# Performance work log

Hardware: AMD Instinct MI355X
Metric: run time of the kernel (lower is better)

Reference implementation:

```python
import jax, jax.numpy as jnp
import numpy as np

T = 16          # timesteps
BATCH = 8       # video clips -> leading dim of x is BATCH*T = 128
C_IN = 768      # fixed by nn.Conv2d(768, redu_dim, 1)
D = 256         # redu_dim
K = 64          # num_centers
H = W = 28
EPS = 1e-12     # torch F.normalize eps


def _conv(x, w, padding):
    # x: [N,C,H,W], w: [O,I,kh,kw]
    return jax.lax.conv_general_dilated(
        x, w, window_strides=(1, 1), padding=padding,
        dimension_numbers=('NCHW', 'OIHW', 'NCHW'))


def setup_inputs() -> dict:
    key = jax.random.key(0)
    ks = jax.random.split(key, 9)
    x = jax.random.normal(ks[0], (BATCH * T, C_IN, H, W), dtype=jnp.float32)
    redu_w = jax.random.normal(ks[1], (D, C_IN, 1, 1), jnp.float32) * 0.02
    redu_b = jnp.zeros((D,), jnp.float32)
    share_w = jax.random.normal(ks[2], (K, D, 1, 1), jnp.float32) * 0.05
    share_b = jnp.zeros((K,), jnp.float32)
    U_z = jax.random.normal(ks[3], (K, K, 3, 3), jnp.float32) * 0.04
    U_r = jax.random.normal(ks[4], (K, K, 3, 3), jnp.float32) * 0.04
    U_h = jax.random.normal(ks[5], (K, K, 3, 3), jnp.float32) * 0.04
    centers = jax.random.normal(ks[6], (K, D), jnp.float32) * 0.06
    return {"x": x, "redu_w": redu_w, "redu_b": redu_b,
            "share_w": share_w, "share_b": share_b,
            "U_z": U_z, "U_r": U_r, "U_h": U_h,
            "centers": centers, "timesteps": T}


def reference(x, redu_w, redu_b, share_w, share_b, U_z, U_r, U_h, centers, timesteps):
    t = timesteps
    bt, _, h, w = x.shape
    b = bt // t
    k = share_w.shape[0]
    d = redu_w.shape[0]

    # channel reduction (1x1 conv)
    xr = _conv(x, redu_w, 'VALID') + redu_b[None, :, None, None]        # [bt,d,h,w]
    # shared assignment logits (1x1 conv)
    wxb = _conv(xr, share_w, 'VALID') + share_b[None, :, None, None]     # [bt,k,h,w]
    wxb = wxb.reshape(b, t, k, h, w).transpose(1, 0, 2, 3, 4)            # [t,b,k,h,w]

    # sequential ConvGRU over timesteps
    h0 = jnp.zeros((b, k, h, w), x.dtype)
    def step(h_tm1, w_t):
        z = jax.nn.sigmoid(w_t + _conv(h_tm1, U_z, 'SAME'))
        r = jax.nn.sigmoid(w_t + _conv(h_tm1, U_r, 'SAME'))
        hh = jnp.tanh(w_t + _conv(r * h_tm1, U_h, 'SAME'))
        h_new = (1.0 - z) * hh + z * h_tm1
        return h_new, h_new
    _, hs = jax.lax.scan(step, h0, wxb)                                  # [t,b,k,h,w]

    assign = hs.transpose(1, 0, 2, 3, 4).reshape(b * t, k, h * w)        # [bt,k,hw]
    # softmax over centers per spatial location
    assign = jax.nn.softmax(assign, axis=1)

    # VLAD aggregation
    a_sum = assign.sum(axis=-1, keepdims=True)                           # [bt,k,1]
    a = a_sum * centers[None]                                            # [bt,k,d]
    xf = xr.reshape(b * t, d, h * w)                                     # [bt,d,hw]
    vlad = jnp.einsum('bkp,bdp->bkd', assign, xf) - a                    # [bt,k,d]

    vlad = vlad.reshape(b, t, k, d).sum(axis=1)                          # [b,k,d]
    # intra-norm over feature dim, then global L2 norm
    vlad = vlad / jnp.maximum(jnp.linalg.norm(vlad, axis=2, keepdims=True), EPS)
    vlad = vlad.reshape(b, k * d)
    vlad = vlad / jnp.maximum(jnp.linalg.norm(vlad, axis=1, keepdims=True), EPS)
    return vlad
```

## Files before the change

### kernel.cpp

```cpp
#include <hip/hip_runtime.h>
#include <hip/hip_bf16.h>

#define T_ 16
#define B_ 8
#define CIN 768
#define D_ 256
#define K_ 64
#define HW 784
#define W_ 28

typedef short short8 __attribute__((ext_vector_type(8)));
typedef short short4v __attribute__((ext_vector_type(4)));
typedef float floatx4 __attribute__((ext_vector_type(4)));
typedef unsigned short ushort_t;

__device__ __forceinline__ unsigned short f2bf(float x) {
    union { float f; unsigned u; } v; v.f = x;
    unsigned u = v.u;
    unsigned r = (u + 0x7fffu + ((u >> 16) & 1u)) >> 16;
    return (unsigned short)r;
}
__device__ __forceinline__ float bf2f(unsigned short h) {
    union { unsigned u; float f; } v; v.u = ((unsigned)h) << 16; return v.f;
}

__device__ __forceinline__ float block_reduce_sum_256(float v) {
    for (int off = 32; off > 0; off >>= 1) v += __shfl_down(v, off, 64);
    __shared__ float red[4];
    __shared__ float tot;
    int lane = threadIdx.x & 63, wid = threadIdx.x >> 6;
    if (lane == 0) red[wid] = v;
    __syncthreads();
    if (threadIdx.x == 0) tot = red[0] + red[1] + red[2] + red[3];
    __syncthreads();
    return tot;
}

__global__ __launch_bounds__(256) void cvt_weights(
    const float* __restrict__ rw, const float* __restrict__ sw,
    const float* __restrict__ Uz, const float* __restrict__ Ur,
    const float* __restrict__ Uh,
    ushort_t* __restrict__ whi, ushort_t* __restrict__ wlo,
    ushort_t* __restrict__ shi, ushort_t* __restrict__ slo,
    ushort_t* __restrict__ azh, ushort_t* __restrict__ azl,
    ushort_t* __restrict__ ahh, ushort_t* __restrict__ ahl)
{
    int i = blockIdx.x * 256 + threadIdx.x;
    const int nR = D_ * CIN;
    const int nS = K_ * D_;
    const int nZR = 128 * 576;
    const int nH = 64 * 576;
    if (i < nR) {
        float x = rw[i];
        unsigned short h = f2bf(x);
        whi[i] = h; wlo[i] = f2bf(x - bf2f(h));
    } else if (i < nR + nS) {
        int j = i - nR;
        float x = sw[j];
        unsigned short h = f2bf(x);
        shi[j] = h; slo[j] = f2bf(x - bf2f(h));
    } else if (i < nR + nS + nZR) {
        int j = i - nR - nS;
        int row = j / 576, kk = j - row * 576;
        int tap = kk >> 6, c = kk & 63;
        const float* U = (row < 64) ? Uz : Ur;
        float x = U[(((size_t)(row & 63)) * 64 + c) * 9 + tap];
        unsigned short h = f2bf(x);
        azh[j] = h; azl[j] = f2bf(x - bf2f(h));
    } else if (i < nR + nS + nZR + nH) {
        int j = i - nR - nS - nZR;
        int row = j / 576, kk = j - row * 576;
        int tap = kk >> 6, c = kk & 63;
        float x = Uh[(((size_t)row) * 64 + c) * 9 + tap];
        unsigned short h = f2bf(x);
        ahh[j] = h; ahl[j] = f2bf(x - bf2f(h));
    }
}

template<int BM, int THR, int KD>
__global__ __launch_bounds__(THR, 4) void mfma_conv1x1(
    const float* __restrict__ X, const ushort_t* __restrict__ Whi,
    const ushort_t* __restrict__ Wlo, const float* __restrict__ bias,
    float* __restrict__ Out)
{
    const int nt = blockIdx.x, bt = blockIdx.z;
    const int p0 = nt * 112;
    const int tid = threadIdx.x, lane = tid & 63, wv = tid >> 6;
    const int li = lane & 15, koff = (lane >> 4) * 8;
    constexpr int NWAVE = THR / 64;
    constexpr int MI = BM / (NWAVE * 16);
    constexpr int NKS = KD / 32;
    constexpr int UPT = (THR == 512) ? 1 : 2;
    const float* Xb = X + (size_t)bt * KD * HW;
    float* Ob = Out + (size_t)bt * BM * HW;

    __shared__ ushort_t lB[2][2][112 * 40];

    floatx4 acc[MI][7];
#pragma unroll
    for (int a = 0; a < MI; ++a)
#pragma unroll
        for (int b = 0; b < 7; ++b) acc[a][b] = (floatx4){0.f, 0.f, 0.f, 0.f};

    float bA[8 * UPT], bB[8 * UPT];
    short8 ahi[MI], alo[MI];

    auto loadB = [&](int k0, float* bb) {
#pragma unroll
        for (int u = 0; u < UPT; ++u) {
            int uu = tid + u * THR;
            if (uu < 448) {
                int j = uu / 112, pp = uu - j * 112;
                const float* xp = Xb + (size_t)(k0 + j * 8) * HW + p0 + pp;
#pragma unroll
                for (int c = 0; c < 8; ++c) bb[u * 8 + c] = xp[(size_t)c * HW];
            }
        }
    };
    auto writeB = [&](const float* bb, int wb) {
#pragma unroll
        for (int u = 0; u < UPT; ++u) {
            int uu = tid + u * THR;
            if (uu < 448) {
                int j = uu / 112, pp = uu - j * 112;
                short8 vh, vl;
#pragma unroll
                for (int c = 0; c < 8; ++c) {
                    unsigned short h = f2bf(bb[u * 8 + c]);
                    vh[c] = (short)h; vl[c] = (short)f2bf(bb[u * 8 + c] - bf2f(h));
                }
                *(short8*)&lB[wb][0][pp * 40 + j * 8] = vh;
                *(short8*)&lB[wb][1][pp * 40 + j * 8] = vl;
            }
        }
    };
    auto loadA = [&](int k0) {
#pragma unroll
        for (int mi = 0; mi < MI; ++mi) {
            int m = wv * (MI * 16) + mi * 16 + li;
            ahi[mi] = *(const short8*)(Whi + (size_t)m * KD + k0 + koff);
            alo[mi] = *(const short8*)(Wlo + (size_t)m * KD + k0 + koff);
        }
    };
    auto domfma = [&](int rb) {
        const ushort_t* bh = &lB[rb][0][0];
        const ushort_t* bl = &lB[rb][1][0];
#pragma unroll
        for (int ni = 0; ni < 7; ++ni) {
            int n = ni * 16 + li;
            short8 bhi = *(const short8*)&bh[n * 40 + koff];
            short8 blo = *(const short8*)&bl[n * 40 + koff];
#pragma unroll
            for (int mi = 0; mi < MI; ++mi) {
                acc[mi][ni] = __builtin_amdgcn_mfma_f32_16x16x32_bf16(ahi[mi], bhi, acc[mi][ni], 0, 0, 0);
                acc[mi][ni] = __builtin_amdgcn_mfma_f32_16x16x32_bf16(ahi[mi], blo, acc[mi][ni], 0, 0, 0);
                acc[mi][ni] = __builtin_amdgcn_mfma_f32_16x16x32_bf16(alo[mi], bhi, acc[mi][ni], 0, 0, 0);
            }
        }
    };

    loadB(0, bA);
    writeB(bA, 0);
    loadB(32, bB);
    __syncthreads();

    for (int ks = 0; ks < NKS; ks += 2) {
        loadA(ks * 32);
        if (ks + 1 < NKS) writeB(bB, 1);
        if (ks + 2 < NKS) loadB((ks + 2) * 32, bA);
        domfma(0);
        __syncthreads();
        loadA((ks + 1) * 32);
        if (ks + 2 < NKS) writeB(bA, 0);
        if (ks + 3 < NKS) loadB((ks + 3) * 32, bB);
        domfma(1);
        __syncthreads();
    }

#pragma unroll
    for (int mi = 0; mi < MI; ++mi) {
        int m0g = wv * (MI * 16) + mi * 16 + ((lane >> 4) << 2);
#pragma unroll
        for (int ni = 0; ni < 7; ++ni) {
            int p = p0 + ni * 16 + li;
#pragma unroll
            for (int r = 0; r < 4; ++r)
                Ob[(size_t)(m0g + r) * HW + p] = acc[mi][ni][r] + bias[m0g + r];
        }
    }
}

__global__ __launch_bounds__(512, 2) void gru_step(
    const ushort_t* __restrict__ hRhi, const ushort_t* __restrict__ hRlo,
    ushort_t* __restrict__ hWhi, ushort_t* __restrict__ hWlo,
    const ushort_t* __restrict__ azh, const ushort_t* __restrict__ azl,
    const ushort_t* __restrict__ ahh, const ushort_t* __restrict__ ahl,
    const float* __restrict__ wxb, float* __restrict__ hs_t, int t)
{
    const int y0 = blockIdx.x, b = blockIdx.y;
    const int tid = threadIdx.x, lane = tid & 63, wv = tid >> 6;
    const int li = lane & 15, koff8 = (lane >> 4) * 8, kq = (lane >> 4) * 4;

    __shared__ ushort_t Hhi[5 * 30 * 72], Hlo[5 * 30 * 72];
    __shared__ ushort_t Rhi[3 * 30 * 72], Rlo[3 * 30 * 72];
    __shared__ float zs[28 * 68];

    {
        const ushort_t* gh = hRhi + (size_t)b * HW * 64;
        const ushort_t* gl = hRlo + (size_t)b * HW * 64;
        for (int e = tid; e < 1200; e += 512) {
            int r = e / 240, rem = e - r * 240;
            int lx = rem >> 3, j = rem & 7;
            int gy = y0 - 2 + r, gx = lx - 1;
            short8 vh = {0,0,0,0,0,0,0,0}, vl = {0,0,0,0,0,0,0,0};
            if (gy >= 0 && gy < 28 && gx >= 0 && gx < 28) {
                size_t go = ((size_t)(gy * 28 + gx)) * 64 + j * 8;
                vh = *(const short8*)(gh + go);
                vl = *(const short8*)(gl + go);
            }
            int lo = (r * 30 + lx) * 72 + j * 8;
            *(short8*)&Hhi[lo] = vh;
            *(short8*)&Hlo[lo] = vl;
        }
        short8 z8 = {0,0,0,0,0,0,0,0};
        for (int e = tid; e < 1620; e += 512) {
            if (e < 810) *(short8*)&Rhi[e * 8] = z8;
            else         *(short8*)&Rlo[(e - 810) * 8] = z8;
        }
    }
    __syncthreads();

    const float* wx = wxb + ((size_t)(b * T_ + t) * K_) * HW;
    const int c0 = li;
    const int c1 = (li < 12) ? 16 + li : 0;

    if (wv < 4) {
        const int kb = wv * 16;
        const ushort_t* Ah = azh + (size_t)(kb + li) * 576;
        const ushort_t* Al = azl + (size_t)(kb + li) * 576;
        floatx4 az[2];
        az[0] = (floatx4){0.f,0.f,0.f,0.f}; az[1] = (floatx4){0.f,0.f,0.f,0.f};
#pragma unroll
        for (int tap = 0; tap < 9; ++tap) {
            const int dy = tap / 3, dx = tap - dy * 3;
#pragma unroll
            for (int ch = 0; ch < 2; ++ch) {
                short8 whi_ = *(const short8*)(Ah + tap * 64 + ch * 32 + koff8);
                short8 wlo_ = *(const short8*)(Al + tap * 64 + ch * 32 + koff8);
                int cb = ch * 32 + koff8;
                int o0 = ((dy + 1) * 30 + c0 + dx) * 72 + cb;
                int o1 = ((dy + 1) * 30 + c1 + dx) * 72 + cb;
                short8 bh0 = *(const short8*)&Hhi[o0];
                short8 bl0 = *(const short8*)&Hlo[o0];
                short8 bh1 = *(const short8*)&Hhi[o1];
                short8 bl1 = *(const short8*)&Hlo[o1];
                az[0] = __builtin_amdgcn_mfma_f32_16x16x32_bf16(whi_, bh0, az[0], 0, 0, 0);
                az[0] = __builtin_amdgcn_mfma_f32_16x16x32_bf16(whi_, bl0, az[0], 0, 0, 0);
                az[0] = __builtin_amdgcn_mfma_f32_16x16x32_bf16(wlo_, bh0, az[0], 0, 0, 0);
                az[1] = __builtin_amdgcn_mfma_f32_16x16x32_bf16(whi_, bh1, az[1], 0, 0, 0);
                az[1] = __builtin_amdgcn_mfma_f32_16x16x32_bf16(whi_, bl1, az[1], 0, 0, 0);
                az[1] = __builtin_amdgcn_mfma_f32_16x16x32_bf16(wlo_, bh1, az[1], 0, 0, 0);
            }
        }
        const int kb4 = kb + kq;
#pragma unroll
        for (int cf = 0; cf < 2; ++cf) {
            int c = cf * 16 + li;
            if (c < 28) {
                floatx4 zv;
#pragma unroll
                for (int r = 0; r < 4; ++r)
                    zv[r] = 1.f / (1.f + __expf(-(wx[(size_t)(kb4 + r) * HW + y0 * 28 + c] + az[cf][r])));
                *(floatx4*)&zs[c * 68 + kb4] = zv;
            }
        }
    } else {
        const int kb = (wv - 4) * 16;
        const ushort_t* Ah = azh + (size_t)(64 + kb + li) * 576;
        const ushort_t* Al = azl + (size_t)(64 + kb + li) * 576;
        floatx4 ar[3][2];
#pragma unroll
        for (int i = 0; i < 3; ++i) {
            ar[i][0] = (floatx4){0.f,0.f,0.f,0.f};
            ar[i][1] = (floatx4){0.f,0.f,0.f,0.f};
        }
#pragma unroll
        for (int tap = 0; tap < 9; ++tap) {
            const int dy = tap / 3, dx = tap - dy * 3;
#pragma unroll
            for (int ch = 0; ch < 2; ++ch) {
                short8 whi_ = *(const short8*)(Ah + tap * 64 + ch * 32 + koff8);
                short8 wlo_ = *(const short8*)(Al + tap * 64 + ch * 32 + koff8);
                int cb = ch * 32 + koff8;
#pragma unroll
                for (int rr = 0; rr < 3; ++rr) {
                    int o0 = ((rr + dy) * 30 + c0 + dx) * 72 + cb;
                    int o1 = ((rr + dy) * 30 + c1 + dx) * 72 + cb;
                    short8 bh0 = *(const short8*)&Hhi[o0];
                    short8 bl0 = *(const short8*)&Hlo[o0];
                    short8 bh1 = *(const short8*)&Hhi[o1];
                    short8 bl1 = *(const short8*)&Hlo[o1];
                    ar[rr][0] = __builtin_amdgcn_mfma_f32_16x16x32_bf16(whi_, bh0, ar[rr][0], 0, 0, 0);
                    ar[rr][0] = __builtin_amdgcn_mfma_f32_16x16x32_bf16(whi_, bl0, ar[rr][0], 0, 0, 0);
                    ar[rr][0] = __builtin_amdgcn_mfma_f32_16x16x32_bf16(wlo_, bh0, ar[rr][0], 0, 0, 0);
                    ar[rr][1] = __builtin_amdgcn_mfma_f32_16x16x32_bf16(whi_, bh1, ar[rr][1], 0, 0, 0);
                    ar[rr][1] = __builtin_amdgcn_mfma_f32_16x16x32_bf16(whi_, bl1, ar[rr][1], 0, 0, 0);
                    ar[rr][1] = __builtin_amdgcn_mfma_f32_16x16x32_bf16(wlo_, bh1, ar[rr][1], 0, 0, 0);
                }
            }
        }
        const int kb4 = kb + kq;
#pragma unroll
        for (int rr = 0; rr < 3; ++rr) {
            int gy = y0 - 1 + rr;
            if (gy < 0 || gy >= 28) continue;
#pragma unroll
            for (int cf = 0; cf < 2; ++cf) {
                int c = cf * 16 + li;
                if (c >= 28) continue;
                short4v ph = *(const short4v*)&Hhi[((rr + 1) * 30 + c + 1) * 72 + kb4];
                short4v pl = *(const short4v*)&Hlo[((rr + 1) * 30 + c + 1) * 72 + kb4];
                short4v vh, vl;
#pragma unroll
                for (int r = 0; r < 4; ++r) {
                    float rv = 1.f / (1.f + __expf(-(wx[(size_t)(kb4 + r) * HW + gy * 28 + c] + ar[rr][cf][r])));
                    float hv = bf2f((unsigned short)ph[r]) + bf2f((unsigned short)pl[r]);
                    float rh = rv * hv;
                    unsigned short h = f2bf(rh);
                    vh[r] = (short)h; vl[r] = (short)f2bf(rh - bf2f(h));
                }
                *(short4v*)&Rhi[(rr * 30 + c + 1) * 72 + kb4] = vh;
                *(short4v*)&Rlo[(rr * 30 + c + 1) * 72 + kb4] = vl;
            }
        }
    }
    __syncthreads();

    if (wv < 4) {
        const int kb = wv * 16;
        const ushort_t* Ah = ahh + (size_t)(kb + li) * 576;
        const ushort_t* Al = ahl + (size_t)(kb + li) * 576;
        floatx4 ac[2];
        ac[0] = (floatx4){0.f,0.f,0.f,0.f}; ac[1] = (floatx4){0.f,0.f,0.f,0.f};
#pragma unroll
        for (int tap = 0; tap < 9; ++tap) {
            const int dy = tap / 3, dx = tap - dy * 3;
#pragma unroll
            for (int ch = 0; ch < 2; ++ch) {
                short8 whi_ = *(const short8*)(Ah + tap * 64 + ch * 32 + koff8);
                short8 wlo_ = *(const short8*)(Al + tap * 64 + ch * 32 + koff8);
                int cb = ch * 32 + koff8;
                int o0 = (dy * 30 + c0 + dx) * 72 + cb;
                int o1 = (dy * 30 + c1 + dx) * 72 + cb;
                short8 bh0 = *(const short8*)&Rhi[o0];
                short8 bl0 = *(const short8*)&Rlo[o0];
                short8 bh1 = *(const short8*)&Rhi[o1];
                short8 bl1 = *(const short8*)&Rlo[o1];
                ac[0] = __builtin_amdgcn_mfma_f32_16x16x32_bf16(whi_, bh0, ac[0], 0, 0, 0);
                ac[0] = __builtin_amdgcn_mfma_f32_16x16x32_bf16(whi_, bl0, ac[0], 0, 0, 0);
                ac[0] = __builtin_amdgcn_mfma_f32_16x16x32_bf16(wlo_, bh0, ac[0], 0, 0, 0);
                ac[1] = __builtin_amdgcn_mfma_f32_16x16x32_bf16(whi_, bh1, ac[1], 0, 0, 0);
                ac[1] = __builtin_amdgcn_mfma_f32_16x16x32_bf16(whi_, bl1, ac[1], 0, 0, 0);
                ac[1] = __builtin_amdgcn_mfma_f32_16x16x32_bf16(wlo_, bh1, ac[1], 0, 0, 0);
            }
        }
        const int kb4 = kb + kq;
        float* hsb = hs_t + (size_t)b * K_ * HW;
#pragma unroll
        for (int cf = 0; cf < 2; ++cf) {
            int c = cf * 16 + li;
            if (c >= 28) continue;
            int p = y0 * 28 + c;
            floatx4 zv = *(const floatx4*)&zs[c * 68 + kb4];
            short4v ph = *(const short4v*)&Hhi[(2 * 30 + c + 1) * 72 + kb4];
            short4v pl = *(const short4v*)&Hlo[(2 * 30 + c + 1) * 72 + kb4];
            short4v vh, vl;
#pragma unroll
            for (int r = 0; r < 4; ++r) {
                int k = kb4 + r;
                float xv = wx[(size_t)k * HW + p] + ac[cf][r];
                float e2 = __expf(2.f * xv);
                float th = 1.f - 2.f / (e2 + 1.f);
                float hp = bf2f((unsigned short)ph[r]) + bf2f((unsigned short)pl[r]);
                float hn = (1.f - zv[r]) * th + zv[r] * hp;
                hsb[(size_t)k * HW + p] = hn;
                unsigned short h = f2bf(hn);
                vh[r] = (short)h; vl[r] = (short)f2bf(hn - bf2f(h));
            }
            size_t o = ((size_t)(b * HW) + p) * 64 + kb4;
            *(short4v*)(hWhi + o) = vh;
            *(short4v*)(hWlo + o) = vl;
        }
    }
}

__global__ __launch_bounds__(256) void softmax_k(float* __restrict__ hs)
{
    int q = blockIdx.x;
    int py = blockIdx.y;
    float* base = hs + (size_t)q * K_ * HW;
    for (int p = py * 392 + threadIdx.x; p < (py + 1) * 392 && p < HW; p += 256) {
        float v[64];
        float m = -1e30f;
#pragma unroll
        for (int k = 0; k < 64; ++k) {
            v[k] = base[(size_t)k * HW + p];
            m = fmaxf(m, v[k]);
        }
        float s = 0.f;
#pragma unroll
        for (int k = 0; k < 64; ++k) {
            v[k] = __expf(v[k] - m);
            s += v[k];
        }
        float inv = 1.f / s;
#pragma unroll
        for (int k = 0; k < 64; ++k)
            base[(size_t)k * HW + p] = v[k] * inv;
    }
}

__global__ __launch_bounds__(256) void vlad_k(const float* __restrict__ assign,
    const float* __restrict__ xr, float* __restrict__ vladt,
    float* __restrict__ asum_bt)
{
    int dt = blockIdx.x, t = blockIdx.y, b = blockIdx.z;
    int q = t * B_ + b, bt = b * T_ + t, d0 = dt * 64;
    const float* ab = assign + (size_t)q * K_ * HW;
    const float* xb = xr + (size_t)bt * D_ * HW;
    __shared__ float As[16][68];
    __shared__ float Xs[16][68];
    int tx = threadIdx.x & 15, ty = threadIdx.x >> 4;
    float acc[4][4] = {{0.f}};
    float pacc[4] = {0.f, 0.f, 0.f, 0.f};

    for (int p0 = 0; p0 < HW; p0 += 16) {
#pragma unroll
        for (int it = 0; it < 4; ++it) {
            int e = threadIdx.x + it * 256;
            int row = e >> 4, pp = e & 15;
            float av_ = ab[(size_t)row * HW + p0 + pp];
            As[pp][row] = av_;
            if (dt == 0) pacc[it] += av_;
            Xs[pp][row] = xb[(size_t)(d0 + row) * HW + p0 + pp];
        }
        __syncthreads();
#pragma unroll
        for (int pp = 0; pp < 16; ++pp) {
            float4 a = *(const float4*)&As[pp][ty * 4];
            float4 xv = *(const float4*)&Xs[pp][tx * 4];
            float av[4] = {a.x, a.y, a.z, a.w};
            float xvv[4] = {xv.x, xv.y, xv.z, xv.w};
#pragma unroll
            for (int r = 0; r < 4; ++r)
#pragma unroll
                for (int s = 0; s < 4; ++s)
                    acc[r][s] = fmaf(av[r], xvv[s], acc[r][s]);
        }
        __syncthreads();
    }
#pragma unroll
    for (int r = 0; r < 4; ++r) {
        int k = ty * 4 + r;
        float4 o = {acc[r][0], acc[r][1], acc[r][2], acc[r][3]};
        *(float4*)&vladt[((size_t)bt * K_ + k) * D_ + d0 + tx * 4] = o;
    }
    if (dt == 0) {
#pragma unroll
        for (int it = 0; it < 4; ++it) {
            float s = pacc[it];
#pragma unroll
            for (int off = 1; off < 16; off <<= 1) s += __shfl_xor(s, off, 16);
            if (tx == 0) asum_bt[(size_t)bt * 64 + ty + it * 16] = s;
        }
    }
}

__global__ __launch_bounds__(256) void norm1_k(const float* __restrict__ vladt,
    const float* __restrict__ asum_bt, const float* __restrict__ centers,
    float* __restrict__ out)
{
    int bid = blockIdx.x; int b = bid >> 6, k = bid & 63; int d = threadIdx.x;
    float acc = 0.f;
#pragma unroll
    for (int t = 0; t < T_; ++t)
        acc += vladt[(((size_t)b * T_ + t) * K_ + k) * D_ + d];
    float asum = 0.f;
#pragma unroll
    for (int t = 0; t < T_; ++t)
        asum += asum_bt[(size_t)(b * T_ + t) * 64 + k];
    acc -= asum * centers[(size_t)k * D_ + d];
    float ss = block_reduce_sum_256(acc * acc);
    float n = fmaxf(sqrtf(ss), 1e-12f);
    out[((size_t)b * K_ + k) * D_ + d] = acc / n;
}

__global__ __launch_bounds__(256) void norm2_k(float* __restrict__ out)
{
    int b = blockIdx.x;
    float* v = out + (size_t)b * (K_ * D_);
    float s = 0.f;
    for (int i = threadIdx.x; i < K_ * D_; i += 256) {
        float x = v[i];
        s = fmaf(x, x, s);
    }
    float tot = block_reduce_sum_256(s);
    float n = fmaxf(sqrtf(tot), 1e-12f);
    for (int i = threadIdx.x; i < K_ * D_; i += 256) v[i] = v[i] / n;
}

extern "C" void kernel_launch(void* const* d_in, const int* in_sizes, int n_in,
                              void* d_out, int out_size, void* d_ws, size_t ws_size,
                              hipStream_t stream)
{
    const float* x       = (const float*)d_in[0];
    const float* redu_w  = (const float*)d_in[1];
    const float* redu_b  = (const float*)d_in[2];
    const float* share_w = (const float*)d_in[3];
    const float* share_b = (const float*)d_in[4];
    const float* Uz      = (const float*)d_in[5];
    const float* Ur      = (const float*)d_in[6];
    const float* Uh      = (const float*)d_in[7];
    const float* centers = (const float*)d_in[8];

    float* ws = (float*)d_ws;
    const size_t SZ_XR   = (size_t)128 * D_ * HW;
    const size_t SZ_WXB  = (size_t)128 * K_ * HW;
    const size_t SZ_HS   = (size_t)T_ * B_ * K_ * HW;
    const size_t SZ_PLANE= (size_t)B_ * K_ * HW;

    float* xr     = ws;
    float* wxb    = xr + SZ_XR;
    float* hs     = wxb + SZ_WXB;
    float* asum_bt= hs + SZ_HS;
    float* wsplit = asum_bt + 8192;
    float* area   = wsplit + 323584;

    ushort_t* whi = (ushort_t*)wsplit;
    ushort_t* wlo = whi + 196608;
    ushort_t* shi = wlo + 196608;
    ushort_t* slo = shi + 16384;
    ushort_t* azh = slo + 16384;
    ushort_t* azl = azh + 73728;
    ushort_t* ahh = azl + 73728;
    ushort_t* ahl = ahh + 36864;

    float* vladt = area;
    ushort_t* st = (ushort_t*)area;
    ushort_t* h0hi = st;
    ushort_t* h0lo = st + SZ_PLANE;
    ushort_t* h1hi = st + 2 * SZ_PLANE;
    ushort_t* h1lo = st + 3 * SZ_PLANE;

    hipMemsetAsync(h0hi, 0, 2 * SZ_PLANE * sizeof(ushort_t), stream);

    cvt_weights<<<dim3((D_ * CIN + K_ * D_ + 128 * 576 + 64 * 576 + 255) / 256),
                  256, 0, stream>>>(redu_w, share_w, Uz, Ur, Uh,
                                    whi, wlo, shi, slo, azh, azl, ahh, ahl);

    mfma_conv1x1<256, 512, CIN><<<dim3(7, 1, 128), 512, 0, stream>>>(x, whi, wlo, redu_b, xr);
    mfma_conv1x1<64, 256, D_><<<dim3(7, 1, 128), 256, 0, stream>>>(xr, shi, slo, share_b, wxb);

    for (int t = 0; t < T_; ++t) {
        const ushort_t* rh_ = (t & 1) ? h1hi : h0hi;
        const ushort_t* rl_ = (t & 1) ? h1lo : h0lo;
        ushort_t* wh_ = (t & 1) ? h0hi : h1hi;
        ushort_t* wl_ = (t & 1) ? h0lo : h1lo;
        gru_step<<<dim3(28, 8), 512, 0, stream>>>(rh_, rl_, wh_, wl_,
                                                  azh, azl, ahh, ahl,
                                                  wxb, hs + (size_t)t * SZ_PLANE, t);
    }

    softmax_k<<<dim3(128, 2), 256, 0, stream>>>(hs);

    vlad_k<<<dim3(4, 16, 8), 256, 0, stream>>>(hs, xr, vladt, asum_bt);
    norm1_k<<<512, 256, 0, stream>>>(vladt, asum_bt, centers, (float*)d_out);
    norm2_k<<<8, 256, 0, stream>>>((float*)d_out);
}
```

Measured before the change: 684.3 us.

## Retile conv1x1 to 256 threads, rebalance GRU step waves, widen softmax grid

The 1x1 conv kernel now always runs with 256 threads, so each wave handles more M rows. Its two-stage software pipeline becomes a simpler single-step double buffer. The GRU step kernel redistributes work so each wave pair computes one of z or r for one of the three rows over 64 output channels, replacing the old split where four waves did z and four did all three r rows. The h-conv gets the same per-wave tiling. Softmax now launches 7x128 blocks of 112 active threads instead of 2 blocks per slice with loops, which raises parallelism but leaves some lanes idle.

```diff
diff --git a/kernel.cpp b/kernel.cpp
--- a/kernel.cpp
+++ b/kernel.cpp
@@ -77,8 +77,8 @@
     }
 }
 
-template<int BM, int THR, int KD>
-__global__ __launch_bounds__(THR, 4) void mfma_conv1x1(
+template<int BM, int KD, int MINW>
+__global__ __launch_bounds__(256, MINW) void mfma_conv1x1(
     const float* __restrict__ X, const ushort_t* __restrict__ Whi,
     const ushort_t* __restrict__ Wlo, const float* __restrict__ bias,
     float* __restrict__ Out)
@@ -86,11 +86,9 @@
     const int nt = blockIdx.x, bt = blockIdx.z;
     const int p0 = nt * 112;
     const int tid = threadIdx.x, lane = tid & 63, wv = tid >> 6;
-    const int li = lane & 15, koff = (lane >> 4) * 8;
-    constexpr int NWAVE = THR / 64;
-    constexpr int MI = BM / (NWAVE * 16);
+    const int li = lane & 15, k8 = (lane >> 4) * 8;
+    constexpr int MI = BM / 64;
     constexpr int NKS = KD / 32;
-    constexpr int UPT = (THR == 512) ? 1 : 2;
     const float* Xb = X + (size_t)bt * KD * HW;
     float* Ob = Out + (size_t)bt * BM * HW;
 
@@ -102,54 +100,56 @@
 #pragma unroll
         for (int b = 0; b < 7; ++b) acc[a][b] = (floatx4){0.f, 0.f, 0.f, 0.f};
 
-    float bA[8 * UPT], bB[8 * UPT];
+    float bb[16];
     short8 ahi[MI], alo[MI];
 
-    auto loadB = [&](int k0, float* bb) {
-#pragma unroll
-        for (int u = 0; u < UPT; ++u) {
-            int uu = tid + u * THR;
-            if (uu < 448) {
-                int j = uu / 112, pp = uu - j * 112;
-                const float* xp = Xb + (size_t)(k0 + j * 8) * HW + p0 + pp;
-#pragma unroll
-                for (int c = 0; c < 8; ++c) bb[u * 8 + c] = xp[(size_t)c * HW];
-            }
+    const int u0j = tid / 112, u0p = tid - u0j * 112;
+    const bool u1v = tid < 192;
+    const int u1j = (tid + 256) / 112, u1p = (tid + 256) - u1j * 112;
+
+    auto loadB = [&](int k0) {
+        const float* xp0 = Xb + (size_t)(k0 + u0j * 8) * HW + p0 + u0p;
+#pragma unroll
+        for (int c = 0; c < 8; ++c) bb[c] = xp0[(size_t)c * HW];
+        if (u1v) {
+            const float* xp1 = Xb + (size_t)(k0 + u1j * 8) * HW + p0 + u1p;
+#pragma unroll
+            for (int c = 0; c < 8; ++c) bb[8 + c] = xp1[(size_t)c * HW];
         }
     };
-    auto writeB = [&](const float* bb, int wb) {
-#pragma unroll
-        for (int u = 0; u < UPT; ++u) {
-            int uu = tid + u * THR;
-            if (uu < 448) {
-                int j = uu / 112, pp = uu - j * 112;
-                short8 vh, vl;
-#pragma unroll
-                for (int c = 0; c < 8; ++c) {
-                    unsigned short h = f2bf(bb[u * 8 + c]);
-                    vh[c] = (short)h; vl[c] = (short)f2bf(bb[u * 8 + c] - bf2f(h));
-                }
-                *(short8*)&lB[wb][0][pp * 40 + j * 8] = vh;
-                *(short8*)&lB[wb][1][pp * 40 + j * 8] = vl;
-            }
+    auto writeB = [&](int wb) {
+        short8 vh, vl;
+#pragma unroll
+        for (int c = 0; c < 8; ++c) {
+            unsigned short h = f2bf(bb[c]);
+            vh[c] = (short)h; vl[c] = (short)f2bf(bb[c] - bf2f(h));
+        }
+        *(short8*)&lB[wb][0][u0p * 40 + u0j * 8] = vh;
+        *(short8*)&lB[wb][1][u0p * 40 + u0j * 8] = vl;
+        if (u1v) {
+#pragma unroll
+            for (int c = 0; c < 8; ++c) {
+                unsigned short h = f2bf(bb[8 + c]);
+                vh[c] = (short)h; vl[c] = (short)f2bf(bb[8 + c] - bf2f(h));
+            }
+            *(short8*)&lB[wb][0][u1p * 40 + u1j * 8] = vh;
+            *(short8*)&lB[wb][1][u1p * 40 + u1j * 8] = vl;
         }
     };
     auto loadA = [&](int k0) {
 #pragma unroll
         for (int mi = 0; mi < MI; ++mi) {
             int m = wv * (MI * 16) + mi * 16 + li;
-            ahi[mi] = *(const short8*)(Whi + (size_t)m * KD + k0 + koff);
-            alo[mi] = *(const short8*)(Wlo + (size_t)m * KD + k0 + koff);
+            ahi[mi] = *(const short8*)(Whi + (size_t)m * KD + k0 + k8);
+            alo[mi] = *(const short8*)(Wlo + (size_t)m * KD + k0 + k8);
         }
     };
     auto domfma = [&](int rb) {
-        const ushort_t* bh = &lB[rb][0][0];
-        const ushort_t* bl = &lB[rb][1][0];
 #pragma unroll
         for (int ni = 0; ni < 7; ++ni) {
             int n = ni * 16 + li;
-            short8 bhi = *(const short8*)&bh[n * 40 + koff];
-            short8 blo = *(const short8*)&bl[n * 40 + koff];
+            short8 bhi = *(const short8*)&lB[rb][0][n * 40 + k8];
+            short8 blo = *(const short8*)&lB[rb][1][n * 40 + k8];
 #pragma unroll
             for (int mi = 0; mi < MI; ++mi) {
                 acc[mi][ni] = __builtin_amdgcn_mfma_f32_16x16x32_bf16(ahi[mi], bhi, acc[mi][ni], 0, 0, 0);
@@ -159,21 +159,16 @@
         }
     };
 
-    loadB(0, bA);
-    writeB(bA, 0);
-    loadB(32, bB);
+    loadB(0);
+    writeB(0);
     __syncthreads();
 
-    for (int ks = 0; ks < NKS; ks += 2) {
+    for (int ks = 0; ks < NKS; ++ks) {
+        int rb = ks & 1;
+        if (ks + 1 < NKS) loadB((ks + 1) * 32);
         loadA(ks * 32);
-        if (ks + 1 < NKS) writeB(bB, 1);
-        if (ks + 2 < NKS) loadB((ks + 2) * 32, bA);
-        domfma(0);
-        __syncthreads();
-        loadA((ks + 1) * 32);
-        if (ks + 2 < NKS) writeB(bA, 0);
-        if (ks + 3 < NKS) loadB((ks + 3) * 32, bB);
-        domfma(1);
+        domfma(rb);
+        if (ks + 1 < NKS) writeB(rb ^ 1);
         __syncthreads();
     }
 
@@ -199,7 +194,7 @@
 {
     const int y0 = blockIdx.x, b = blockIdx.y;
     const int tid = threadIdx.x, lane = tid & 63, wv = tid >> 6;
-    const int li = lane & 15, koff8 = (lane >> 4) * 8, kq = (lane >> 4) * 4;
+    const int li = lane & 15, k8 = (lane >> 4) * 8, kq = (lane >> 4) * 4;
 
     __shared__ ushort_t Hhi[5 * 30 * 72], Hlo[5 * 30 * 72];
     __shared__ ushort_t Rhi[3 * 30 * 72], Rlo[3 * 30 * 72];
@@ -231,154 +226,117 @@
     __syncthreads();
 
     const float* wx = wxb + ((size_t)(b * T_ + t) * K_) * HW;
-    const int c0 = li;
-    const int c1 = (li < 12) ? 16 + li : 0;
-
-    if (wv < 4) {
-        const int kb = wv * 16;
-        const ushort_t* Ah = azh + (size_t)(kb + li) * 576;
-        const ushort_t* Al = azl + (size_t)(kb + li) * 576;
-        floatx4 az[2];
-        az[0] = (floatx4){0.f,0.f,0.f,0.f}; az[1] = (floatx4){0.f,0.f,0.f,0.f};
+
+    {
+        const int g = wv >> 1;
+        const int nf = wv & 1;
+        const int c = nf * 16 + li;
+        const bool cv = (c < 28);
+        const int cc = cv ? c : 0;
+        const int arow0 = (g == 0) ? 0 : 64;
+        const int rowoff = (g == 0) ? 1 : (g - 1);
+
+        floatx4 a4[4];
+#pragma unroll
+        for (int mi = 0; mi < 4; ++mi) a4[mi] = (floatx4){0.f,0.f,0.f,0.f};
+
 #pragma unroll
         for (int tap = 0; tap < 9; ++tap) {
             const int dy = tap / 3, dx = tap - dy * 3;
+            const int hrow = ((rowoff + dy) * 30 + cc + dx) * 72;
 #pragma unroll
             for (int ch = 0; ch < 2; ++ch) {
-                short8 whi_ = *(const short8*)(Ah + tap * 64 + ch * 32 + koff8);
-                short8 wlo_ = *(const short8*)(Al + tap * 64 + ch * 32 + koff8);
-                int cb = ch * 32 + koff8;
-                int o0 = ((dy + 1) * 30 + c0 + dx) * 72 + cb;
-                int o1 = ((dy + 1) * 30 + c1 + dx) * 72 + cb;
-                short8 bh0 = *(const short8*)&Hhi[o0];
-                short8 bl0 = *(const short8*)&Hlo[o0];
-                short8 bh1 = *(const short8*)&Hhi[o1];
-                short8 bl1 = *(const short8*)&Hlo[o1];
-                az[0] = __builtin_amdgcn_mfma_f32_16x16x32_bf16(whi_, bh0, az[0], 0, 0, 0);
-                az[0] = __builtin_amdgcn_mfma_f32_16x16x32_bf16(whi_, bl0, az[0], 0, 0, 0);
-                az[0] = __builtin_amdgcn_mfma_f32_16x16x32_bf16(wlo_, bh0, az[0], 0, 0, 0);
-                az[1] = __builtin_amdgcn_mfma_f32_16x16x32_bf16(whi_, bh1, az[1], 0, 0, 0);
-                az[1] = __builtin_amdgcn_mfma_f32_16x16x32_bf16(whi_, bl1, az[1], 0, 0, 0);
-                az[1] = __builtin_amdgcn_mfma_f32_16x16x32_bf16(wlo_, bh1, az[1], 0, 0, 0);
-            }
-        }
-        const int kb4 = kb + kq;
-#pragma unroll
-        for (int cf = 0; cf < 2; ++cf) {
-            int c = cf * 16 + li;
-            if (c < 28) {
-                floatx4 zv;
-#pragma unroll
-                for (int r = 0; r < 4; ++r)
-                    zv[r] = 1.f / (1.f + __expf(-(wx[(size_t)(kb4 + r) * HW + y0 * 28 + c] + az[cf][r])));
-                *(floatx4*)&zs[c * 68 + kb4] = zv;
-            }
-        }
-    } else {
-        const int kb = (wv - 4) * 16;
-        const ushort_t* Ah = azh + (size_t)(64 + kb + li) * 576;
-        const ushort_t* Al = azl + (size_t)(64 + kb + li) * 576;
-        floatx4 ar[3][2];
-#pragma unroll
-        for (int i = 0; i < 3; ++i) {
-            ar[i][0] = (floatx4){0.f,0.f,0.f,0.f};
-            ar[i][1] = (floatx4){0.f,0.f,0.f,0.f};
-        }
+                const int hb = hrow + ch * 32 + k8;
+                short8 bh = *(const short8*)&Hhi[hb];
+                short8 bl = *(const short8*)&Hlo[hb];
+                const int acol = tap * 64 + ch * 32 + k8;
+#pragma unroll
+                for (int mi = 0; mi < 4; ++mi) {
+                    int ar = arow0 + mi * 16 + li;
+                    short8 wh = *(const short8*)(azh + (size_t)ar * 576 + acol);
+                    short8 wl = *(const short8*)(azl + (size_t)ar * 576 + acol);
+                    a4[mi] = __builtin_amdgcn_mfma_f32_16x16x32_bf16(wh, bh, a4[mi], 0, 0, 0);
+                    a4[mi] = __builtin_amdgcn_mfma_f32_16x16x32_bf16(wh, bl, a4[mi], 0, 0, 0);
+                    a4[mi] = __builtin_amdgcn_mfma_f32_16x16x32_bf16(wl, bh, a4[mi], 0, 0, 0);
+                }
+            }
+        }
+
+        if (g == 0) {
+            if (cv) {
+#pragma unroll
+                for (int mi = 0; mi < 4; ++mi) {
+                    int kb4 = mi * 16 + kq;
+                    floatx4 zv;
+#pragma unroll
+                    for (int r = 0; r < 4; ++r)
+                        zv[r] = 1.f / (1.f + __expf(-(wx[(size_t)(kb4 + r) * HW + y0 * 28 + c] + a4[mi][r])));
+                    *(floatx4*)&zs[c * 68 + kb4] = zv;
+                }
+            }
+        } else {
+            const int rr = g - 1, gy = y0 - 1 + rr;
+            if (cv && gy >= 0 && gy < 28) {
+#pragma unroll
+                for (int mi = 0; mi < 4; ++mi) {
+                    int kb4 = mi * 16 + kq;
+                    short4v ph = *(const short4v*)&Hhi[((rr + 1) * 30 + c + 1) * 72 + kb4];
+                    short4v pl = *(const short4v*)&Hlo[((rr + 1) * 30 + c + 1) * 72 + kb4];
+                    short4v vh, vl;
+#pragma unroll
+                    for (int r = 0; r < 4; ++r) {
+                        float rv = 1.f / (1.f + __expf(-(wx[(size_t)(kb4 + r) * HW + gy * 28 + c] + a4[mi][r])));
+                        float hv = bf2f((unsigned short)ph[r]) + bf2f((unsigned short)pl[r]);
+                        float rh = rv * hv;
+                        unsigned short h = f2bf(rh);
+                        vh[r] = (short)h; vl[r] = (short)f2bf(rh - bf2f(h));
+                    }
+                    *(short4v*)&Rhi[(rr * 30 + c + 1) * 72 + kb4] = vh;
+                    *(short4v*)&Rlo[(rr * 30 + c + 1) * 72 + kb4] = vl;
+                }
+            }
+        }
+    }
+    __syncthreads();
+
+    {
+        const int mi2 = wv >> 1, nf2 = wv & 1;
+        const int c2 = nf2 * 16 + li;
+        const bool c2v = (c2 < 28);
+        const int cc2 = c2v ? c2 : 0;
+
+        floatx4 a1 = (floatx4){0.f,0.f,0.f,0.f};
 #pragma unroll
         for (int tap = 0; tap < 9; ++tap) {
             const int dy = tap / 3, dx = tap - dy * 3;
+            const int rrow = (dy * 30 + cc2 + dx) * 72;
 #pragma unroll
             for (int ch = 0; ch < 2; ++ch) {
-                short8 whi_ = *(const short8*)(Ah + tap * 64 + ch * 32 + koff8);
-                short8 wlo_ = *(const short8*)(Al + tap * 64 + ch * 32 + koff8);
-                int cb = ch * 32 + koff8;
-#pragma unroll
-                for (int rr = 0; rr < 3; ++rr) {
-                    int o0 = ((rr + dy) * 30 + c0 + dx) * 72 + cb;
-                    int o1 = ((rr + dy) * 30 + c1 + dx) * 72 + cb;
-                    short8 bh0 = *(const short8*)&Hhi[o0];
-                    short8 bl0 = *(const short8*)&Hlo[o0];
-                    short8 bh1 = *(const short8*)&Hhi[o1];
-                    short8 bl1 = *(const short8*)&Hlo[o1];
-                    ar[rr][0] = __builtin_amdgcn_mfma_f32_16x16x32_bf16(whi_, bh0, ar[rr][0], 0, 0, 0);
-                    ar[rr][0] = __builtin_amdgcn_mfma_f32_16x16x32_bf16(whi_, bl0, ar[rr][0], 0, 0, 0);
-                    ar[rr][0] = __builtin_amdgcn_mfma_f32_16x16x32_bf16(wlo_, bh0, ar[rr][0], 0, 0, 0);
-                    ar[rr][1] = __builtin_amdgcn_mfma_f32_16x16x32_bf16(whi_, bh1, ar[rr][1], 0, 0, 0);
-                    ar[rr][1] = __builtin_amdgcn_mfma_f32_16x16x32_bf16(whi_, bl1, ar[rr][1], 0, 0, 0);
-                    ar[rr][1] = __builtin_amdgcn_mfma_f32_16x16x32_bf16(wlo_, bh1, ar[rr][1], 0, 0, 0);
-                }
-            }
-        }
-        const int kb4 = kb + kq;
-#pragma unroll
-        for (int rr = 0; rr < 3; ++rr) {
-            int gy = y0 - 1 + rr;
-            if (gy < 0 || gy >= 28) continue;
-#pragma unroll
-            for (int cf = 0; cf < 2; ++cf) {
-                int c = cf * 16 + li;
-                if (c >= 28) continue;
-                short4v ph = *(const short4v*)&Hhi[((rr + 1) * 30 + c + 1) * 72 + kb4];
-                short4v pl = *(const short4v*)&Hlo[((rr + 1) * 30 + c + 1) * 72 + kb4];
-                short4v vh, vl;
-#pragma unroll
-                for (int r = 0; r < 4; ++r) {
-                    float rv = 1.f / (1.f + __expf(-(wx[(size_t)(kb4 + r) * HW + gy * 28 + c] + ar[rr][cf][r])));
-                    float hv = bf2f((unsigned short)ph[r]) + bf2f((unsigned short)pl[r]);
-                    float rh = rv * hv;
-                    unsigned short h = f2bf(rh);
-                    vh[r] = (short)h; vl[r] = (short)f2bf(rh - bf2f(h));
-                }
-                *(short4v*)&Rhi[(rr * 30 + c + 1) * 72 + kb4] = vh;
-                *(short4v*)&Rlo[(rr * 30 + c + 1) * 72 + kb4] = vl;
-            }
-        }
-    }
-    __syncthreads();
-
-    if (wv < 4) {
-        const int kb = wv * 16;
-        const ushort_t* Ah = ahh + (size_t)(kb + li) * 576;
-        const ushort_t* Al = ahl + (size_t)(kb + li) * 576;
-        floatx4 ac[2];
-        ac[0] = (floatx4){0.f,0.f,0.f,0.f}; ac[1] = (floatx4){0.f,0.f,0.f,0.f};
-#pragma unroll
-        for (int tap = 0; tap < 9; ++tap) {
-            const int dy = tap / 3, dx = tap - dy * 3;
-#pragma unroll
-            for (int ch = 0; ch < 2; ++ch) {
-                short8 whi_ = *(const short8*)(Ah + tap * 64 + ch * 32 + koff8);
-                short8 wlo_ = *(const short8*)(Al + tap * 64 + ch * 32 + koff8);
-                int cb = ch * 32 + koff8;
-                int o0 = (dy * 30 + c0 + dx) * 72 + cb;
-                int o1 = (dy * 30 + c1 + dx) * 72 + cb;
-                short8 bh0 = *(const short8*)&Rhi[o0];
-                short8 bl0 = *(const short8*)&Rlo[o0];
-                short8 bh1 = *(const short8*)&Rhi[o1];
-                short8 bl1 = *(const short8*)&Rlo[o1];
-                ac[0] = __builtin_amdgcn_mfma_f32_16x16x32_bf16(whi_, bh0, ac[0], 0, 0, 0);
-                ac[0] = __builtin_amdgcn_mfma_f32_16x16x32_bf16(whi_, bl0, ac[0], 0, 0, 0);
-                ac[0] = __builtin_amdgcn_mfma_f32_16x16x32_bf16(wlo_, bh0, ac[0], 0, 0, 0);
-                ac[1] = __builtin_amdgcn_mfma_f32_16x16x32_bf16(whi_, bh1, ac[1], 0, 0, 0);
-                ac[1] = __builtin_amdgcn_mfma_f32_16x16x32_bf16(whi_, bl1, ac[1], 0, 0, 0);
-                ac[1] = __builtin_amdgcn_mfma_f32_16x16x32_bf16(wlo_, bh1, ac[1], 0, 0, 0);
-            }
-        }
-        const int kb4 = kb + kq;
-        float* hsb = hs_t + (size_t)b * K_ * HW;
-#pragma unroll
-        for (int cf = 0; cf < 2; ++cf) {
-            int c = cf * 16 + li;
-            if (c >= 28) continue;
-            int p = y0 * 28 + c;
-            floatx4 zv = *(const floatx4*)&zs[c * 68 + kb4];
-            short4v ph = *(const short4v*)&Hhi[(2 * 30 + c + 1) * 72 + kb4];
-            short4v pl = *(const short4v*)&Hlo[(2 * 30 + c + 1) * 72 + kb4];
+                const int rb = rrow + ch * 32 + k8;
+                short8 bh = *(const short8*)&Rhi[rb];
+                short8 bl = *(const short8*)&Rlo[rb];
+                const int acol = tap * 64 + ch * 32 + k8;
+                int ar = mi2 * 16 + li;
+                short8 wh = *(const short8*)(ahh + (size_t)ar * 576 + acol);
+                short8 wl = *(const short8*)(ahl + (size_t)ar * 576 + acol);
+                a1 = __builtin_amdgcn_mfma_f32_16x16x32_bf16(wh, bh, a1, 0, 0, 0);
+                a1 = __builtin_amdgcn_mfma_f32_16x16x32_bf16(wh, bl, a1, 0, 0, 0);
+                a1 = __builtin_amdgcn_mfma_f32_16x16x32_bf16(wl, bh, a1, 0, 0, 0);
+            }
+        }
+
+        if (c2v) {
+            const int kb4 = mi2 * 16 + kq;
+            const int p = y0 * 28 + c2;
+            float* hsb = hs_t + (size_t)b * K_ * HW;
+            floatx4 zv = *(const floatx4*)&zs[c2 * 68 + kb4];
+            short4v ph = *(const short4v*)&Hhi[(2 * 30 + c2 + 1) * 72 + kb4];
+            short4v pl = *(const short4v*)&Hlo[(2 * 30 + c2 + 1) * 72 + kb4];
             short4v vh, vl;
 #pragma unroll
             for (int r = 0; r < 4; ++r) {
                 int k = kb4 + r;
-                float xv = wx[(size_t)k * HW + p] + ac[cf][r];
+                float xv = wx[(size_t)k * HW + p] + a1[r];
                 float e2 = __expf(2.f * xv);
                 float th = 1.f - 2.f / (e2 + 1.f);
                 float hp = bf2f((unsigned short)ph[r]) + bf2f((unsigned short)pl[r]);
@@ -394,30 +352,29 @@
     }
 }
 
-__global__ __launch_bounds__(256) void softmax_k(float* __restrict__ hs)
+__global__ __launch_bounds__(128) void softmax_k(float* __restrict__ hs)
 {
     int q = blockIdx.x;
-    int py = blockIdx.y;
+    int p = blockIdx.y * 112 + threadIdx.x;
+    if (threadIdx.x >= 112) return;
     float* base = hs + (size_t)q * K_ * HW;
-    for (int p = py * 392 + threadIdx.x; p < (py + 1) * 392 && p < HW; p += 256) {
-        float v[64];
-        float m = -1e30f;
-#pragma unroll
-        for (int k = 0; k < 64; ++k) {
-            v[k] = base[(size_t)k * HW + p];
-            m = fmaxf(m, v[k]);
-        }
-        float s = 0.f;
-#pragma unroll
-        for (int k = 0; k < 64; ++k) {
-            v[k] = __expf(v[k] - m);
-            s += v[k];
-        }
-        float inv = 1.f / s;
-#pragma unroll
-        for (int k = 0; k < 64; ++k)
-            base[(size_t)k * HW + p] = v[k] * inv;
-    }
+    float v[64];
+    float m = -1e30f;
+#pragma unroll
+    for (int k = 0; k < 64; ++k) {
+        v[k] = base[(size_t)k * HW + p];
+        m = fmaxf(m, v[k]);
+    }
+    float s = 0.f;
+#pragma unroll
+    for (int k = 0; k < 64; ++k) {
+        v[k] = __expf(v[k] - m);
+        s += v[k];
+    }
+    float inv = 1.f / s;
+#pragma unroll
+    for (int k = 0; k < 64; ++k)
+        base[(size_t)k * HW + p] = v[k] * inv;
 }
 
 __global__ __launch_bounds__(256) void vlad_k(const float* __restrict__ assign,
@@ -558,8 +515,8 @@
                   256, 0, stream>>>(redu_w, share_w, Uz, Ur, Uh,
                                     whi, wlo, shi, slo, azh, azl, ahh, ahl);
 
-    mfma_conv1x1<256, 512, CIN><<<dim3(7, 1, 128), 512, 0, stream>>>(x, whi, wlo, redu_b, xr);
-    mfma_conv1x1<64, 256, D_><<<dim3(7, 1, 128), 256, 0, stream>>>(xr, shi, slo, share_b, wxb);
+    mfma_conv1x1<256, CIN, 2><<<dim3(7, 1, 128), 256, 0, stream>>>(x, whi, wlo, redu_b, xr);
+    mfma_conv1x1<64, D_, 4><<<dim3(7, 1, 128), 256, 0, stream>>>(xr, shi, slo, share_b, wxb);
 
     for (int t = 0; t < T_; ++t) {
         const ushort_t* rh_ = (t & 1) ? h1hi : h0hi;
@@ -571,7 +528,7 @@
                                                   wxb, hs + (size_t)t * SZ_PLANE, t);
     }
 
-    softmax_k<<<dim3(128, 2), 256, 0, stream>>>(hs);
+    softmax_k<<<dim3(128, 7), 128, 0, stream>>>(hs);
 
     vlad_k<<<dim3(4, 16, 8), 256, 0, stream>>>(hs, xr, vladt, asum_bt);
     norm1_k<<<512, 256, 0, stream>>>(vladt, asum_bt, centers, (float*)d_out);
```

New measurement: 1.059 ms. 1.55x slower.
